# Performance work log

Hardware: AMD Instinct MI355X
Metric: run time of the kernel (lower is better)

## Reference

```python
import jax, jax.numpy as jnp
import numpy as np

DIM = 512; H = 8; TEMP_LEN = 16; TARGET_LEN = 22
NT = TEMP_LEN ** 2          # 256 temp tokens
NS = TARGET_LEN ** 2        # 484 target tokens
N = NT + NS                 # 740
HD = DIM // H
SCALE = HD ** -0.5
EPS = 1e-5
B = 16


def _bias_index(L):
    coords = np.stack(np.meshgrid(np.arange(L), np.arange(L), indexing='ij')).reshape(2, -1)
    rel = (coords[:, :, None] - coords[:, None, :]).transpose(1, 2, 0)  # [L^2, L^2, 2]
    rel[..., 0] += L - 1
    rel[..., 1] += L - 1
    rel[..., 0] *= 2 * L - 1
    return jnp.asarray(rel.sum(-1))  # [L^2, L^2] indices into (2L-1)^2 table

TEMP_IDX = _bias_index(TEMP_LEN)
TARGET_IDX = _bias_index(TARGET_LEN)


def setup_inputs() -> dict:
    key = jax.random.key(0)
    ctr = iter(range(100))
    def nrm(shape, s=1.0):
        return jax.random.normal(jax.random.fold_in(key, next(ctr)), shape, jnp.float32) * s
    def uni(shape):
        return jax.random.uniform(jax.random.fold_in(key, next(ctr)), shape, jnp.float32, 0.5, 1.5)
    d = {'x': nrm((B, N, DIM))}
    for nm in ('q', 'k', 'v'):
        d[f'conv_{nm}_w'] = nrm((DIM, 1, 3, 3), 0.2)   # depthwise 3x3, groups=DIM
        d[f'bn_{nm}_g'] = 1.0 + nrm((DIM,), 0.1)
        d[f'bn_{nm}_b'] = nrm((DIM,), 0.1)
        d[f'bn_{nm}_m'] = nrm((DIM,), 0.1)
        d[f'bn_{nm}_v'] = uni((DIM,))
    for nm in ('q', 'k', 'v', 'p'):
        d[f'w{nm}'] = nrm((DIM, DIM), DIM ** -0.5)
        d[f'b{nm}'] = nrm((DIM,), 0.01)
    d['rpb_target'] = nrm(((2 * TARGET_LEN - 1) ** 2, H), 0.0002)
    d['rpb_temp'] = nrm(((2 * TEMP_LEN - 1) ** 2, 1), 0.0002)
    d['tt_bias'] = nrm((H, 1, NT), 0.0002)       # temp_target_bias_table
    d['tg_tm_bias'] = nrm((H, NS, 1), 0.0002)    # target_temp_bias_table
    return d


def _dwconv_bn(z, w, g, b, m, v):
    # z: [B, C, Hh, Ww]; depthwise conv + BatchNorm2d (inference stats)
    y = jax.lax.conv_general_dilated(z, w, (1, 1), ((1, 1), (1, 1)),
                                     dimension_numbers=('NCHW', 'OIHW', 'NCHW'),
                                     feature_group_count=DIM)
    inv = (g * jax.lax.rsqrt(v + EPS))[None, :, None, None]
    return (y - m[None, :, None, None]) * inv + b[None, :, None, None]


def reference(x, conv_q_w, bn_q_g, bn_q_b, bn_q_m, bn_q_v,
              conv_k_w, bn_k_g, bn_k_b, bn_k_m, bn_k_v,
              conv_v_w, bn_v_g, bn_v_b, bn_v_m, bn_v_v,
              wq, bq, wk, bk, wv, bv, wp, bp,
              rpb_target, rpb_temp, tt_bias, tg_tm_bias):
    Bb = x.shape[0]
    to_img = lambda t, L: t.transpose(0, 2, 1).reshape(Bb, DIM, L, L)
    to_seq = lambda t: t.reshape(Bb, DIM, -1).transpose(0, 2, 1)
    ti = to_img(x[:, :NT], TEMP_LEN)
    tg = to_img(x[:, NT:], TARGET_LEN)

    def conv_branch(w, g, b, m, v):
        return jnp.concatenate([to_seq(_dwconv_bn(ti, w, g, b, m, v)),
                                to_seq(_dwconv_bn(tg, w, g, b, m, v))], axis=1)

    q = conv_branch(conv_q_w, bn_q_g, bn_q_b, bn_q_m, bn_q_v) @ wq + bq
    k = conv_branch(conv_k_w, bn_k_g, bn_k_b, bn_k_m, bn_k_v) @ wk + bk
    v = conv_branch(conv_v_w, bn_v_g, bn_v_b, bn_v_m, bn_v_v) @ wv + bv

    heads = lambda t: t.reshape(Bb, -1, H, HD).transpose(0, 2, 1, 3)
    qtm, ktm, vtm = heads(q[:, :NT]), heads(k[:, :NT]), heads(v[:, :NT])
    qta, kh, vh = heads(q[:, NT:]), heads(k), heads(v)

    # gathered relative-position bias tables
    target_bias = rpb_target[TARGET_IDX.reshape(-1)].reshape(NS, NS, H).transpose(2, 0, 1)  # [H,NS,NS]
    temp_bias = rpb_temp[TEMP_IDX.reshape(-1)].reshape(NT, NT, 1).transpose(2, 0, 1)        # [1,NT,NT]
    padding = tt_bias + tg_tm_bias                                                          # [H,NS,NT]
    rel = jnp.concatenate([padding, target_bias], axis=2)                                   # [H,NS,N]

    # target -> all attention
    attn = jax.nn.softmax(jnp.einsum('bhqd,bhkd->bhqk', qta, kh) * SCALE + rel, axis=-1)
    out_t = jnp.einsum('bhqk,bhkd->bhqd', attn, vh).transpose(0, 2, 1, 3).reshape(Bb, NS, DIM)

    # temp -> temp attention (bias broadcast over heads)
    attn2 = jax.nn.softmax(jnp.einsum('bhqd,bhkd->bhqk', qtm, ktm) * SCALE + temp_bias, axis=-1)
    out_m = jnp.einsum('bhqk,bhkd->bhqd', attn2, vtm).transpose(0, 2, 1, 3).reshape(Bb, NT, DIM)

    return jnp.concatenate([out_m, out_t], axis=1) @ wp + bp
```

## Files before the change

kernel.cpp:

```cpp
#include <hip/hip_runtime.h>
#include <hip/hip_bf16.h>

typedef unsigned short u16;
typedef unsigned int u32;
typedef __attribute__((ext_vector_type(8))) short short8;
typedef __attribute__((ext_vector_type(4))) float f32x4;

#define NTOK 740
#define NTMP 256
#define NTGT 484
#define DM   512
#define MH   8
#define MROWS 11840
#define KPAD 768
#define LOG2E 1.4426950408889634f

__device__ __forceinline__ float b2f(u16 u) {
    union { unsigned int i; float f; } x; x.i = ((unsigned int)u) << 16; return x.f;
}
__device__ __forceinline__ u16 f2b(float f) {
    union { float f; unsigned int i; } x; x.f = f;
    unsigned int r = x.i + 0x7FFFu + ((x.i >> 16) & 1u);
    return (u16)(r >> 16);
}
__device__ __forceinline__ u32 pk2(float a, float b) {
    union { __hip_bfloat162 h; u32 u; } p;
    p.h = __float22bfloat162_rn(float2{a, b});
    return p.u;
}
__device__ __forceinline__ float fexp2(float x) {
    return __builtin_amdgcn_exp2f(x);
}
struct alignas(8) us4 { u16 x, y, z, w; };

__device__ __forceinline__ void gload16(const void* g, void* l) {
    __builtin_amdgcn_global_load_lds(
        (const __attribute__((address_space(1))) void*)g,
        (__attribute__((address_space(3))) void*)l, 16, 0, 0);
}

__global__ __launch_bounds__(256) void prep_all(
    const float* __restrict__ w0, const float* __restrict__ w1,
    const float* __restrict__ w2, const float* __restrict__ w3, u16* __restrict__ wTbase,
    const float* __restrict__ cw0, const float* __restrict__ g0, const float* __restrict__ bb0,
    const float* __restrict__ m0, const float* __restrict__ v0,
    const float* __restrict__ cw1, const float* __restrict__ g1, const float* __restrict__ bb1,
    const float* __restrict__ m1, const float* __restrict__ v1,
    const float* __restrict__ cw2, const float* __restrict__ g2, const float* __restrict__ bb2,
    const float* __restrict__ m2, const float* __restrict__ v2,
    float* __restrict__ cwfb, float* __restrict__ shb,
    const float* __restrict__ rpb_t, const float* __restrict__ tt,
    const float* __restrict__ tg, u16* __restrict__ btab,
    const float* __restrict__ rpb_m, u16* __restrict__ mtab) {
    __shared__ float t[32][33];
    const int id = blockIdx.x, tid = threadIdx.x;
    if (id < 1024) {
        const int z = id >> 8, rem = id & 255;
        const int bx = rem & 15, by = rem >> 4;
        const float* W = z == 0 ? w0 : z == 1 ? w1 : z == 2 ? w2 : w3;
        u16* WT = wTbase + (size_t)z * 262144;
        const int tx = tid & 31, ty = tid >> 5;
        for (int i = ty; i < 32; i += 8)
            t[i][tx] = W[(size_t)(by * 32 + i) * 512 + bx * 32 + tx];
        __syncthreads();
        for (int i = ty; i < 32; i += 8)
            WT[(size_t)(bx * 32 + i) * 512 + by * 32 + tx] = f2b(t[tx][i]);
    } else if (id < 1051) {
        const int rem = id - 1024;
        const int tap = rem % 9, br = rem / 9;
        const float* cw = br == 0 ? cw0 : br == 1 ? cw1 : cw2;
        const float* g  = br == 0 ? g0  : br == 1 ? g1  : g2;
        const float* bb = br == 0 ? bb0 : br == 1 ? bb1 : bb2;
        const float* m  = br == 0 ? m0  : br == 1 ? m1  : m2;
        const float* v  = br == 0 ? v0  : br == 1 ? v1  : v2;
        for (int c = tid; c < DM; c += 256) {
            const float inv = g[c] * rsqrtf(v[c] + 1e-5f);
            cwfb[(br * 9 + tap) * DM + c] = cw[c * 9 + tap] * inv;
            if (tap == 0) shb[br * DM + c] = bb[c] - m[c] * inv;
        }
    } else if (id < 4923) {
        const int rem = id - 1051;
        const int h = rem / NTGT, q = rem % NTGT;
        const int qh = q / 22, qw = q % 22;
        const float tgv = tg[h * NTGT + q];
        for (int k = tid; k < KPAD; k += 256) {
            float val;
            if (k < NTMP) val = (tt[h * NTMP + k] + tgv) * LOG2E;
            else if (k < NTOK) {
                const int kj = k - NTMP, kh = kj / 22, kw = kj % 22;
                val = rpb_t[((qh - kh + 21) * 43 + (qw - kw + 21)) * MH + h] * LOG2E;
            } else val = -1e30f;
            btab[((size_t)(h * NTGT + q)) * KPAD + k] = f2b(val);
        }
    } else {
        const int q = id - 4923, k = tid;
        const int qh = q >> 4, qw = q & 15, kh = k >> 4, kw = k & 15;
        mtab[q * 256 + k] = f2b(rpb_m[(qh - kh + 15) * 31 + (qw - kw + 15)] * LOG2E);
    }
}

__global__ __launch_bounds__(256) void conv_bn3(
    const float* __restrict__ x,
    const float* __restrict__ cwfb, const float* __restrict__ shb,
    u16* __restrict__ o0, u16* __restrict__ o1, u16* __restrict__ o2) {
    const int bn = blockIdx.x * 2 + (threadIdx.x >> 7);
    const int c = (threadIdx.x & 127) * 4;
    const int b = bn / NTOK, n = bn % NTOK;
    const bool tmp = n < NTMP;
    const int L = tmp ? 16 : 22, base = tmp ? 0 : NTMP, p = n - base;
    const int ph = p / L, pw = p % L;
    float4 xv[9];
#pragma unroll
    for (int tap = 0; tap < 9; ++tap) {
        const int dh = tap / 3 - 1, dw = tap % 3 - 1;
        const int h2 = ph + dh, w2 = pw + dw;
        const bool ok = (h2 >= 0 && h2 < L && w2 >= 0 && w2 < L);
        xv[tap] = ok ? *(const float4*)(x + (size_t)(b * NTOK + base + h2 * L + w2) * DM + c)
                     : float4{0.f, 0.f, 0.f, 0.f};
    }
    const size_t o = (size_t)bn * DM + c;
    u16* out[3] = {o0, o1, o2};
#pragma unroll
    for (int br = 0; br < 3; ++br) {
        float4 acc = *(const float4*)(shb + br * DM + c);
#pragma unroll
        for (int tap = 0; tap < 9; ++tap) {
            const float4 wv = *(const float4*)(cwfb + (br * 9 + tap) * DM + c);
            acc.x = fmaf(wv.x, xv[tap].x, acc.x);
            acc.y = fmaf(wv.y, xv[tap].y, acc.y);
            acc.z = fmaf(wv.z, xv[tap].z, acc.z);
            acc.w = fmaf(wv.w, xv[tap].w, acc.w);
        }
        us4 r;
        r.x = f2b(acc.x); r.y = f2b(acc.y); r.z = f2b(acc.z); r.w = f2b(acc.w);
        *(us4*)(out[br] + o) = r;
    }
}

#define STAGE(bf, kk) do {                                                           \
    gload16(asrc + (kk) * 32, &As[bf][w * 512]);                                     \
    gload16(bsrc0 + (kk) * 32, &Bs[bf][w * 1024]);                                   \
    gload16(bsrc1 + (kk) * 32, &Bs[bf][w * 1024 + 512]);                             \
} while (0)

#define GEMM_BODY(A, BT)                                                             \
    const int tid = threadIdx.x;                                                     \
    const int lane = tid & 63, w = tid >> 6;                                         \
    const int lr = lane & 15, lg = lane >> 4;                                        \
    const int wm = (w >> 1) * 32, wn = (w & 1) * 64;                                 \
    const int srow4 = lane >> 2;                                                     \
    const int sc = (lane & 3) ^ ((srow4 & 3) ^ ((srow4 >> 2) & 3));                  \
    const int flr = (lr & 3) ^ ((lr >> 2) & 3);                                      \
    const u16* asrc  = A  + (size_t)(gm0 + w * 16 + srow4) * 512 + sc * 8;           \
    const u16* bsrc0 = BT + (size_t)(gn0 + w * 32 + srow4) * 512 + sc * 8;           \
    const u16* bsrc1 = BT + (size_t)(gn0 + w * 32 + 16 + srow4) * 512 + sc * 8;      \
    f32x4 acc[2][4] = {};                                                            \
    STAGE(0, 0); STAGE(1, 1);                                                        \
    _Pragma("unroll")                                                                \
    for (int kt = 0; kt < 16; ++kt) {                                                \
        const int cur = kt % 3;                                                      \
        if (kt < 14) {                                                               \
            STAGE((kt + 2) % 3, kt + 2);                                             \
            asm volatile("s_waitcnt vmcnt(6)" ::: "memory");                         \
        } else if (kt == 14) {                                                       \
            asm volatile("s_waitcnt vmcnt(3)" ::: "memory");                         \
        } else {                                                                     \
            asm volatile("s_waitcnt vmcnt(0)" ::: "memory");                         \
        }                                                                            \
        __builtin_amdgcn_s_barrier();                                                \
        asm volatile("" ::: "memory");                                               \
        short8 af[2], bfr[4];                                                        \
        _Pragma("unroll")                                                            \
        for (int i = 0; i < 2; ++i)                                                  \
            af[i] = *(const short8*)&As[cur][(wm + i * 16 + lr) * 32 + (lg ^ flr) * 8]; \
        _Pragma("unroll")                                                            \
        for (int j = 0; j < 4; ++j)                                                  \
            bfr[j] = *(const short8*)&Bs[cur][(wn + j * 16 + lr) * 32 + (lg ^ flr) * 8]; \
        _Pragma("unroll")                                                            \
        for (int i = 0; i < 2; ++i)                                                  \
            _Pragma("unroll")                                                        \
            for (int j = 0; j < 4; ++j)                                              \
                acc[i][j] = __builtin_amdgcn_mfma_f32_16x16x32_bf16(af[i], bfr[j], acc[i][j], 0, 0, 0); \
        asm volatile("" ::: "memory");                                               \
        __builtin_amdgcn_s_barrier();                                                \
    }

__global__ __launch_bounds__(256) void gemm_qkv(
    const u16* __restrict__ Aq, const u16* __restrict__ Ak, const u16* __restrict__ Av,
    const u16* __restrict__ wTb, const float* __restrict__ bq,
    const float* __restrict__ bk, const float* __restrict__ bv,
    u16* __restrict__ qout, u16* __restrict__ kout, u16* __restrict__ vbT, int zbase) {
    __shared__ u16 As[3][2048];
    __shared__ u16 Bs[3][4096];
    const int gm0 = blockIdx.x * 64, gn0 = blockIdx.y * 128;
    const int z = blockIdx.z + zbase;
    const u16* A = z == 0 ? Aq : z == 1 ? Ak : Av;
    const u16* BT = wTb + (size_t)z * 262144;
    const float* bias = z == 0 ? bq : z == 1 ? bk : bv;
    GEMM_BODY(A, BT)
    u16* lin = z == 0 ? qout : kout;
#pragma unroll
    for (int i = 0; i < 2; ++i)
#pragma unroll
        for (int j = 0; j < 4; ++j) {
            const int gc = gn0 + wn + j * 16 + lr;
            const float bvl = bias[gc];
#pragma unroll
            for (int r = 0; r < 4; ++r) {
                const int gr = gm0 + wm + i * 16 + lg * 4 + r;
                const float val = acc[i][j][r] + bvl;
                if (z == 2) {
                    const int b2 = gr / NTOK, k = gr - b2 * NTOK;
                    const int hh = gc >> 6, d = gc & 63;
                    vbT[((size_t)(b2 * MH + hh) * 64 + d) * KPAD + k] = f2b(val);
                } else {
                    lin[(size_t)gr * 512 + gc] = f2b(val);
                }
            }
        }
}

__global__ __launch_bounds__(256) void gemm_out(const u16* __restrict__ Ain,
                                                const u16* __restrict__ BTin,
                                                const float* __restrict__ bias,
                                                float* __restrict__ C) {
    __shared__ u16 As[3][2048];
    __shared__ u16 Bs[3][4096];
    const int gm0 = blockIdx.x * 64, gn0 = blockIdx.y * 128;
    GEMM_BODY(Ain, BTin)
#pragma unroll
    for (int i = 0; i < 2; ++i)
#pragma unroll
        for (int j = 0; j < 4; ++j) {
            const int gc = gn0 + wn + j * 16 + lr;
            const float bvl = bias[gc];
#pragma unroll
            for (int r = 0; r < 4; ++r) {
                const int gr = gm0 + wm + i * 16 + lg * 4 + r;
                C[(size_t)gr * 512 + gc] = acc[i][j][r] + bvl;
            }
        }
}

__global__ __launch_bounds__(256) void attn_all(const u16* __restrict__ qb,
                                                const u16* __restrict__ kb,
                                                const u16* __restrict__ vbT,
                                                const u16* __restrict__ btab,
                                                const u16* __restrict__ mtab,
                                                u16* __restrict__ attb) {
    __shared__ u16 Ks[2][32][64];
    __shared__ u16 VTs[2][64][32];
    __shared__ u16 Pb[2][4][16][32];

    int wg = blockIdx.x + 6 * (blockIdx.y + 8 * blockIdx.z);
    wg = (wg & 7) * 96 + (wg >> 3);
    const int bx = wg % 6;
    const int hb = wg / 6;
    const int h = hb & 7, b = hb >> 3;

    const bool tgt = bx < 4;
    const int q0 = (tgt ? bx : bx - 4) * 128;
    const int NKr = tgt ? NTOK : NTMP;
    const int NCH = tgt ? 24 : 8;
    const int QTOT = tgt ? NTGT : NTMP;
    const int QOFF = tgt ? NTMP : 0;
    const int TK = tgt ? KPAD : 256;
    const int tid = threadIdx.x;
    const int w = tid >> 6, lane = tid & 63;
    const int lq = lane & 15, lg = lane >> 4;
    const int fq = (lq & 3) ^ ((lq >> 2) & 3);
    const size_t brow = (size_t)b * NTOK;
    const float SCL = 0.125f * LOG2E;

    int qA = q0 + w * 16 + lq;       if (qA > QTOT - 1) qA = QTOT - 1;
    int qB = q0 + 64 + w * 16 + lq;  if (qB > QTOT - 1) qB = QTOT - 1;
    const u16* tbase = tgt ? (btab + (size_t)h * NTGT * KPAD) : mtab;
    const u16* trowA = tbase + (size_t)qA * TK;
    const u16* trowB = tbase + (size_t)qB * TK;

    short8 qfA[2], qfB[2];
#pragma unroll
    for (int dc = 0; dc < 2; ++dc) {
        qfA[dc] = *(const short8*)(qb + (brow + QOFF + qA) * DM + h * 64 + dc * 32 + lg * 8);
        qfB[dc] = *(const short8*)(qb + (brow + QOFF + qB) * DM + h * 64 + dc * 32 + lg * 8);
    }

    const int krow = tid >> 3, ksc = tid & 7;
    const int vrow = tid >> 2, vsc = tid & 3;
    const int fv = (vrow & 3) ^ ((vrow >> 2) & 3);
    const size_t vbase = (size_t)(b * MH + h) * 64 * KPAD;
    const u16* kptr2 = kb + brow * DM + h * 64 + (ksc ^ (krow & 7)) * 8;
    const u16* vptr2 = vbT + vbase + (size_t)vrow * KPAD + (vsc ^ fv) * 8;
    const int NKm1 = NKr - 1;

    float mrunA = -1e30f, lrunA = 0.f, mrunB = -1e30f, lrunB = 0.f;
    f32x4 oTA[4] = {}, oTB[4] = {};

    {
        const int keyc = krow < NKm1 ? krow : NKm1;
        gload16(kptr2 + (size_t)keyc * DM, &Ks[0][w * 8][0]);
        gload16(vptr2, &VTs[0][w * 16][0]);
    }

    for (int kc = 0; kc < NCH; ++kc) {
        const int cur = kc & 1, nxt = cur ^ 1;
        const bool more = (kc + 1 < NCH);
        us4 bcA0 = *(const us4*)(trowA + kc * 32 + lg * 4);
        us4 bcA1 = *(const us4*)(trowA + kc * 32 + 16 + lg * 4);
        us4 bcB0 = *(const us4*)(trowB + kc * 32 + lg * 4);
        us4 bcB1 = *(const us4*)(trowB + kc * 32 + 16 + lg * 4);
        if (more) {
            const int key = (kc + 1) * 32 + krow;
            const int keyc = key < NKm1 ? key : NKm1;
            gload16(kptr2 + (size_t)keyc * DM, &Ks[nxt][w * 8][0]);
            gload16(vptr2 + (kc + 1) * 32, &VTs[nxt][w * 16][0]);
            asm volatile("s_waitcnt vmcnt(2)" ::: "memory");
        } else {
            asm volatile("s_waitcnt vmcnt(0)" ::: "memory");
        }
        __builtin_amdgcn_s_barrier();
        asm volatile("" ::: "memory");

        f32x4 sA0 = {}, sA1 = {}, sB0 = {}, sB1 = {};
        __builtin_amdgcn_s_setprio(1);
#pragma unroll
        for (int dc = 0; dc < 2; ++dc) {
            short8 a0 = *(const short8*)&Ks[cur][lq][((dc * 4 + lg) ^ (lq & 7)) * 8];
            short8 a1 = *(const short8*)&Ks[cur][16 + lq][((dc * 4 + lg) ^ (lq & 7)) * 8];
            sA0 = __builtin_amdgcn_mfma_f32_16x16x32_bf16(a0, qfA[dc], sA0, 0, 0, 0);
            sB0 = __builtin_amdgcn_mfma_f32_16x16x32_bf16(a0, qfB[dc], sB0, 0, 0, 0);
            sA1 = __builtin_amdgcn_mfma_f32_16x16x32_bf16(a1, qfA[dc], sA1, 0, 0, 0);
            sB1 = __builtin_amdgcn_mfma_f32_16x16x32_bf16(a1, qfB[dc], sB1, 0, 0, 0);
        }
        __builtin_amdgcn_s_setprio(0);

        {
            float sv[8];
            sv[0] = fmaf(sA0[0], SCL, b2f(bcA0.x)); sv[1] = fmaf(sA0[1], SCL, b2f(bcA0.y));
            sv[2] = fmaf(sA0[2], SCL, b2f(bcA0.z)); sv[3] = fmaf(sA0[3], SCL, b2f(bcA0.w));
            sv[4] = fmaf(sA1[0], SCL, b2f(bcA1.x)); sv[5] = fmaf(sA1[1], SCL, b2f(bcA1.y));
            sv[6] = fmaf(sA1[2], SCL, b2f(bcA1.z)); sv[7] = fmaf(sA1[3], SCL, b2f(bcA1.w));
            float cm = sv[0];
#pragma unroll
            for (int i = 1; i < 8; ++i) cm = fmaxf(cm, sv[i]);
            cm = fmaxf(cm, __shfl_xor(cm, 16));
            cm = fmaxf(cm, __shfl_xor(cm, 32));
            if (!__all(cm <= mrunA)) {
                const float mnew = fmaxf(mrunA, cm);
                const float alpha = fexp2(mrunA - mnew);
#pragma unroll
                for (int t = 0; t < 4; ++t)
#pragma unroll
                    for (int r = 0; r < 4; ++r) oTA[t][r] *= alpha;
                lrunA *= alpha;
                mrunA = mnew;
            }
            float pv[8], psum = 0.f;
#pragma unroll
            for (int i = 0; i < 8; ++i) { pv[i] = fexp2(sv[i] - mrunA); psum += pv[i]; }
            const int c0 = (((lg >> 1) ^ fq) & 3) * 8 + (lg & 1) * 4;
            const int c1 = (((2 + (lg >> 1)) ^ fq) & 3) * 8 + (lg & 1) * 4;
            *(uint2*)&Pb[0][w][lq][c0] = uint2{pk2(pv[0], pv[1]), pk2(pv[2], pv[3])};
            *(uint2*)&Pb[0][w][lq][c1] = uint2{pk2(pv[4], pv[5]), pk2(pv[6], pv[7])};
            psum += __shfl_xor(psum, 16);
            psum += __shfl_xor(psum, 32);
            lrunA += psum;
        }
        {
            float sv[8];
            sv[0] = fmaf(sB0[0], SCL, b2f(bcB0.x)); sv[1] = fmaf(sB0[1], SCL, b2f(bcB0.y));
            sv[2] = fmaf(sB0[2], SCL, b2f(bcB0.z)); sv[3] = fmaf(sB0[3], SCL, b2f(bcB0.w));
            sv[4] = fmaf(sB1[0], SCL, b2f(bcB1.x)); sv[5] = fmaf(sB1[1], SCL, b2f(bcB1.y));
            sv[6] = fmaf(sB1[2], SCL, b2f(bcB1.z)); sv[7] = fmaf(sB1[3], SCL, b2f(bcB1.w));
            float cm = sv[0];
#pragma unroll
            for (int i = 1; i < 8; ++i) cm = fmaxf(cm, sv[i]);
            cm = fmaxf(cm, __shfl_xor(cm, 16));
            cm = fmaxf(cm, __shfl_xor(cm, 32));
            if (!__all(cm <= mrunB)) {
                const float mnew = fmaxf(mrunB, cm);
                const float alpha = fexp2(mrunB - mnew);
#pragma unroll
                for (int t = 0; t < 4; ++t)
#pragma unroll
                    for (int r = 0; r < 4; ++r) oTB[t][r] *= alpha;
                lrunB *= alpha;
                mrunB = mnew;
            }
            float pv[8], psum = 0.f;
#pragma unroll
            for (int i = 0; i < 8; ++i) { pv[i] = fexp2(sv[i] - mrunB); psum += pv[i]; }
            const int c0 = (((lg >> 1) ^ fq) & 3) * 8 + (lg & 1) * 4;
            const int c1 = (((2 + (lg >> 1)) ^ fq) & 3) * 8 + (lg & 1) * 4;
            *(uint2*)&Pb[1][w][lq][c0] = uint2{pk2(pv[0], pv[1]), pk2(pv[2], pv[3])};
            *(uint2*)&Pb[1][w][lq][c1] = uint2{pk2(pv[4], pv[5]), pk2(pv[6], pv[7])};
            psum += __shfl_xor(psum, 16);
            psum += __shfl_xor(psum, 32);
            lrunB += psum;
        }

        asm volatile("s_waitcnt lgkmcnt(0)" ::: "memory");

        short8 pfA = *(const short8*)&Pb[0][w][lq][((lg ^ fq) & 3) * 8];
        short8 pfB = *(const short8*)&Pb[1][w][lq][((lg ^ fq) & 3) * 8];
        __builtin_amdgcn_s_setprio(1);
#pragma unroll
        for (int t = 0; t < 4; ++t) {
            short8 vf = *(const short8*)&VTs[cur][t * 16 + lq][((lg ^ fq) & 3) * 8];
            oTA[t] = __builtin_amdgcn_mfma_f32_16x16x32_bf16(vf, pfA, oTA[t], 0, 0, 0);
            oTB[t] = __builtin_amdgcn_mfma_f32_16x16x32_bf16(vf, pfB, oTB[t], 0, 0, 0);
        }
        __builtin_amdgcn_s_setprio(0);

        asm volatile("" ::: "memory");
        __builtin_amdgcn_s_barrier();
    }

    {
        const float linv = 1.f / lrunA;
        const int qrow = q0 + w * 16 + lq;
        if (qrow < QTOT) {
            u16* op = attb + (brow + QOFF + qrow) * DM + h * 64;
#pragma unroll
            for (int t = 0; t < 4; ++t)
                *(uint2*)(op + t * 16 + lg * 4) =
                    uint2{pk2(oTA[t][0] * linv, oTA[t][1] * linv),
                          pk2(oTA[t][2] * linv, oTA[t][3] * linv)};
        }
    }
    {
        const float linv = 1.f / lrunB;
        const int qrow = q0 + 64 + w * 16 + lq;
        if (qrow < QTOT) {
            u16* op = attb + (brow + QOFF + qrow) * DM + h * 64;
#pragma unroll
            for (int t = 0; t < 4; ++t)
                *(uint2*)(op + t * 16 + lg * 4) =
                    uint2{pk2(oTB[t][0] * linv, oTB[t][1] * linv),
                          pk2(oTB[t][2] * linv, oTB[t][3] * linv)};
        }
    }
}

extern "C" void kernel_launch(void* const* d_in, const int* in_sizes, int n_in,
                              void* d_out, int out_size, void* d_ws, size_t ws_size,
                              hipStream_t stream) {
    const float* x = (const float*)d_in[0];
    const float* convw[3] = {(const float*)d_in[1], (const float*)d_in[6], (const float*)d_in[11]};
    const float* bng[3]   = {(const float*)d_in[2], (const float*)d_in[7], (const float*)d_in[12]};
    const float* bnb[3]   = {(const float*)d_in[3], (const float*)d_in[8], (const float*)d_in[13]};
    const float* bnm[3]   = {(const float*)d_in[4], (const float*)d_in[9], (const float*)d_in[14]};
    const float* bnv[3]   = {(const float*)d_in[5], (const float*)d_in[10], (const float*)d_in[15]};
    const float* w[4]     = {(const float*)d_in[16], (const float*)d_in[18], (const float*)d_in[20], (const float*)d_in[22]};
    const float* bias[4]  = {(const float*)d_in[17], (const float*)d_in[19], (const float*)d_in[21], (const float*)d_in[23]};
    const float* rpb_t = (const float*)d_in[24];
    const float* rpb_m = (const float*)d_in[25];
    const float* tt    = (const float*)d_in[26];
    const float* tg    = (const float*)d_in[27];

    char* p = (char*)d_ws;
    auto alloc = [&](size_t n) { char* r = p; p += (n + 255) & ~(size_t)255; return r; };
    const size_t SEQ = (size_t)MROWS * DM * 2;
    u16* wTb  = (u16*)alloc(4 * 524288);
    u16* cbq  = (u16*)alloc(SEQ);
    u16* cbk  = (u16*)alloc(SEQ);
    u16* cbv  = (u16*)alloc(SEQ);
    u16* kbuf = (u16*)alloc(SEQ);
    u16* vbT  = (u16*)alloc((size_t)16 * MH * 64 * KPAD * 2);
    u16* btab = (u16*)alloc((size_t)MH * NTGT * KPAD * 2);
    u16* mtab = (u16*)alloc(256 * 256 * 2);
    float* cwf = (float*)alloc(3 * 9 * DM * 4);
    float* shf = (float*)alloc(3 * DM * 4);
    const size_t used = (size_t)(p - (char*)d_ws);
    const bool merged = ws_size >= used + SEQ;
    u16* qbuf = merged ? (u16*)alloc(SEQ) : cbv;
    u16* attb = cbq;

    prep_all<<<5179, 256, 0, stream>>>(
        w[0], w[1], w[2], w[3], wTb,
        convw[0], bng[0], bnb[0], bnm[0], bnv[0],
        convw[1], bng[1], bnb[1], bnm[1], bnv[1],
        convw[2], bng[2], bnb[2], bnm[2], bnv[2], cwf, shf,
        rpb_t, tt, tg, btab, rpb_m, mtab);

    conv_bn3<<<MROWS / 2, 256, 0, stream>>>(x, cwf, shf, cbq, cbk, cbv);

    if (merged) {
        gemm_qkv<<<dim3(185, 4, 3), 256, 0, stream>>>(cbq, cbk, cbv, wTb,
                                                      bias[0], bias[1], bias[2],
                                                      qbuf, kbuf, vbT, 0);
    } else {
        gemm_qkv<<<dim3(185, 4, 1), 256, 0, stream>>>(cbq, cbk, cbv, wTb,
                                                      bias[0], bias[1], bias[2],
                                                      qbuf, kbuf, vbT, 2);
        gemm_qkv<<<dim3(185, 4, 2), 256, 0, stream>>>(cbq, cbk, cbv, wTb,
                                                      bias[0], bias[1], bias[2],
                                                      qbuf, kbuf, vbT, 0);
    }

    attn_all<<<dim3(6, 8, 16), 256, 0, stream>>>(qbuf, kbuf, vbT, btab, mtab, attb);

    gemm_out<<<dim3(185, 4), 256, 0, stream>>>(attb, wTb + 3 * 262144, bias[3], (float*)d_out);
}
```

Measured before the change: 171.3 us.

## Split target-query attention over two key halves and merge partial softmax results

Target-query attention blocks are split into two workgroups, each covering half of the key chunks (12 of 24). Each writes fp32 partial max, sum and output to workspace, and a new combine kernel merges them with log-sum-exp rescaling. This raises the grid from 768 to 1280 workgroups and balances the long target blocks against the short temp blocks, aiming for better CU occupancy and less tail time. The cost is an extra kernel launch plus roughly 19 MB of fp32 partial traffic. The split path only runs when the workspace is large enough, otherwise the old kernel is used.

```diff
diff --git a/kernel.cpp b/kernel.cpp
--- a/kernel.cpp
+++ b/kernel.cpp
@@ -242,6 +242,264 @@
         }
 }
 
+#define ATTN_CORE(BC_A0, BC_A1, BC_B0, BC_B1)                                        \
+    f32x4 sA0 = {}, sA1 = {}, sB0 = {}, sB1 = {};                                    \
+    __builtin_amdgcn_s_setprio(1);                                                   \
+    _Pragma("unroll")                                                                \
+    for (int dc = 0; dc < 2; ++dc) {                                                 \
+        short8 a0 = *(const short8*)&Ks[cur][lq][((dc * 4 + lg) ^ (lq & 7)) * 8];    \
+        short8 a1 = *(const short8*)&Ks[cur][16 + lq][((dc * 4 + lg) ^ (lq & 7)) * 8]; \
+        sA0 = __builtin_amdgcn_mfma_f32_16x16x32_bf16(a0, qfA[dc], sA0, 0, 0, 0);    \
+        sB0 = __builtin_amdgcn_mfma_f32_16x16x32_bf16(a0, qfB[dc], sB0, 0, 0, 0);    \
+        sA1 = __builtin_amdgcn_mfma_f32_16x16x32_bf16(a1, qfA[dc], sA1, 0, 0, 0);    \
+        sB1 = __builtin_amdgcn_mfma_f32_16x16x32_bf16(a1, qfB[dc], sB1, 0, 0, 0);    \
+    }                                                                                \
+    __builtin_amdgcn_s_setprio(0);                                                   \
+    {                                                                                \
+        float sv[8];                                                                 \
+        sv[0] = fmaf(sA0[0], SCL, b2f(BC_A0.x)); sv[1] = fmaf(sA0[1], SCL, b2f(BC_A0.y)); \
+        sv[2] = fmaf(sA0[2], SCL, b2f(BC_A0.z)); sv[3] = fmaf(sA0[3], SCL, b2f(BC_A0.w)); \
+        sv[4] = fmaf(sA1[0], SCL, b2f(BC_A1.x)); sv[5] = fmaf(sA1[1], SCL, b2f(BC_A1.y)); \
+        sv[6] = fmaf(sA1[2], SCL, b2f(BC_A1.z)); sv[7] = fmaf(sA1[3], SCL, b2f(BC_A1.w)); \
+        float cm = sv[0];                                                            \
+        _Pragma("unroll")                                                            \
+        for (int i = 1; i < 8; ++i) cm = fmaxf(cm, sv[i]);                           \
+        cm = fmaxf(cm, __shfl_xor(cm, 16));                                          \
+        cm = fmaxf(cm, __shfl_xor(cm, 32));                                          \
+        if (!__all(cm <= mrunA)) {                                                   \
+            const float mnew = fmaxf(mrunA, cm);                                     \
+            const float alpha = fexp2(mrunA - mnew);                                 \
+            _Pragma("unroll")                                                        \
+            for (int t = 0; t < 4; ++t)                                              \
+                _Pragma("unroll")                                                    \
+                for (int r = 0; r < 4; ++r) oTA[t][r] *= alpha;                      \
+            lrunA *= alpha;                                                          \
+            mrunA = mnew;                                                            \
+        }                                                                            \
+        float pv[8], psum = 0.f;                                                     \
+        _Pragma("unroll")                                                            \
+        for (int i = 0; i < 8; ++i) { pv[i] = fexp2(sv[i] - mrunA); psum += pv[i]; } \
+        const int c0 = (((lg >> 1) ^ fq) & 3) * 8 + (lg & 1) * 4;                    \
+        const int c1 = (((2 + (lg >> 1)) ^ fq) & 3) * 8 + (lg & 1) * 4;              \
+        *(uint2*)&Pb[0][w][lq][c0] = uint2{pk2(pv[0], pv[1]), pk2(pv[2], pv[3])};    \
+        *(uint2*)&Pb[0][w][lq][c1] = uint2{pk2(pv[4], pv[5]), pk2(pv[6], pv[7])};    \
+        psum += __shfl_xor(psum, 16);                                                \
+        psum += __shfl_xor(psum, 32);                                                \
+        lrunA += psum;                                                               \
+    }                                                                                \
+    {                                                                                \
+        float sv[8];                                                                 \
+        sv[0] = fmaf(sB0[0], SCL, b2f(BC_B0.x)); sv[1] = fmaf(sB0[1], SCL, b2f(BC_B0.y)); \
+        sv[2] = fmaf(sB0[2], SCL, b2f(BC_B0.z)); sv[3] = fmaf(sB0[3], SCL, b2f(BC_B0.w)); \
+        sv[4] = fmaf(sB1[0], SCL, b2f(BC_B1.x)); sv[5] = fmaf(sB1[1], SCL, b2f(BC_B1.y)); \
+        sv[6] = fmaf(sB1[2], SCL, b2f(BC_B1.z)); sv[7] = fmaf(sB1[3], SCL, b2f(BC_B1.w)); \
+        float cm = sv[0];                                                            \
+        _Pragma("unroll")                                                            \
+        for (int i = 1; i < 8; ++i) cm = fmaxf(cm, sv[i]);                           \
+        cm = fmaxf(cm, __shfl_xor(cm, 16));                                          \
+        cm = fmaxf(cm, __shfl_xor(cm, 32));                                          \
+        if (!__all(cm <= mrunB)) {                                                   \
+            const float mnew = fmaxf(mrunB, cm);                                     \
+            const float alpha = fexp2(mrunB - mnew);                                 \
+            _Pragma("unroll")                                                        \
+            for (int t = 0; t < 4; ++t)                                              \
+                _Pragma("unroll")                                                    \
+                for (int r = 0; r < 4; ++r) oTB[t][r] *= alpha;                      \
+            lrunB *= alpha;                                                          \
+            mrunB = mnew;                                                            \
+        }                                                                            \
+        float pv[8], psum = 0.f;                                                     \
+        _Pragma("unroll")                                                            \
+        for (int i = 0; i < 8; ++i) { pv[i] = fexp2(sv[i] - mrunB); psum += pv[i]; } \
+        const int c0 = (((lg >> 1) ^ fq) & 3) * 8 + (lg & 1) * 4;                    \
+        const int c1 = (((2 + (lg >> 1)) ^ fq) & 3) * 8 + (lg & 1) * 4;              \
+        *(uint2*)&Pb[1][w][lq][c0] = uint2{pk2(pv[0], pv[1]), pk2(pv[2], pv[3])};    \
+        *(uint2*)&Pb[1][w][lq][c1] = uint2{pk2(pv[4], pv[5]), pk2(pv[6], pv[7])};    \
+        psum += __shfl_xor(psum, 16);                                                \
+        psum += __shfl_xor(psum, 32);                                                \
+        lrunB += psum;                                                               \
+    }                                                                                \
+    asm volatile("s_waitcnt lgkmcnt(0)" ::: "memory");                               \
+    {                                                                                \
+        short8 pfA = *(const short8*)&Pb[0][w][lq][((lg ^ fq) & 3) * 8];             \
+        short8 pfB = *(const short8*)&Pb[1][w][lq][((lg ^ fq) & 3) * 8];             \
+        __builtin_amdgcn_s_setprio(1);                                               \
+        _Pragma("unroll")                                                            \
+        for (int t = 0; t < 4; ++t) {                                                \
+            short8 vf = *(const short8*)&VTs[cur][t * 16 + lq][((lg ^ fq) & 3) * 8]; \
+            oTA[t] = __builtin_amdgcn_mfma_f32_16x16x32_bf16(vf, pfA, oTA[t], 0, 0, 0); \
+            oTB[t] = __builtin_amdgcn_mfma_f32_16x16x32_bf16(vf, pfB, oTB[t], 0, 0, 0); \
+        }                                                                            \
+        __builtin_amdgcn_s_setprio(0);                                               \
+    }
+
+__global__ __launch_bounds__(256) void attn_split(const u16* __restrict__ qb,
+                                                  const u16* __restrict__ kb,
+                                                  const u16* __restrict__ vbT,
+                                                  const u16* __restrict__ btab,
+                                                  const u16* __restrict__ mtab,
+                                                  u16* __restrict__ attb,
+                                                  float* __restrict__ pm,
+                                                  float* __restrict__ pl,
+                                                  float* __restrict__ pO) {
+    __shared__ u16 Ks[2][32][64];
+    __shared__ u16 VTs[2][64][32];
+    __shared__ u16 Pb[2][4][16][32];
+
+    int wg = blockIdx.x + 10 * (blockIdx.y + 8 * blockIdx.z);
+    wg = (wg & 7) * 160 + (wg >> 3);
+    const int bx = wg % 10;
+    const int hb = wg / 10;
+    const int h = hb & 7, b = hb >> 3;
+
+    const bool tgt = bx < 8;
+    const int half = tgt ? (bx & 1) : 0;
+    const int q0 = tgt ? (bx >> 1) * 128 : (bx - 8) * 128;
+    const int NKr = tgt ? NTOK : NTMP;
+    const int gc0 = tgt ? half * 12 : 0;
+    const int gcEnd = tgt ? gc0 + 12 : 8;
+    const int QTOT = tgt ? NTGT : NTMP;
+    const int QOFF = tgt ? NTMP : 0;
+    const int TK = tgt ? KPAD : 256;
+    const int tid = threadIdx.x;
+    const int w = tid >> 6, lane = tid & 63;
+    const int lq = lane & 15, lg = lane >> 4;
+    const int fq = (lq & 3) ^ ((lq >> 2) & 3);
+    const size_t brow = (size_t)b * NTOK;
+    const float SCL = 0.125f * LOG2E;
+
+    int qA = q0 + w * 16 + lq;       if (qA > QTOT - 1) qA = QTOT - 1;
+    int qB = q0 + 64 + w * 16 + lq;  if (qB > QTOT - 1) qB = QTOT - 1;
+    const u16* tbase = tgt ? (btab + (size_t)h * NTGT * KPAD) : mtab;
+    const u16* trowA = tbase + (size_t)qA * TK;
+    const u16* trowB = tbase + (size_t)qB * TK;
+
+    short8 qfA[2], qfB[2];
+#pragma unroll
+    for (int dc = 0; dc < 2; ++dc) {
+        qfA[dc] = *(const short8*)(qb + (brow + QOFF + qA) * DM + h * 64 + dc * 32 + lg * 8);
+        qfB[dc] = *(const short8*)(qb + (brow + QOFF + qB) * DM + h * 64 + dc * 32 + lg * 8);
+    }
+
+    const int krow = tid >> 3, ksc = tid & 7;
+    const int vrow = tid >> 2, vsc = tid & 3;
+    const int fv = (vrow & 3) ^ ((vrow >> 2) & 3);
+    const size_t vbase = (size_t)(b * MH + h) * 64 * KPAD;
+    const u16* kptr2 = kb + brow * DM + h * 64 + (ksc ^ (krow & 7)) * 8;
+    const u16* vptr2 = vbT + vbase + (size_t)vrow * KPAD + (vsc ^ fv) * 8;
+    const int NKm1 = NKr - 1;
+
+    float mrunA = -1e30f, lrunA = 0.f, mrunB = -1e30f, lrunB = 0.f;
+    f32x4 oTA[4] = {}, oTB[4] = {};
+
+    {
+        const int key = gc0 * 32 + krow;
+        const int keyc = key < NKm1 ? key : NKm1;
+        gload16(kptr2 + (size_t)keyc * DM, &Ks[0][w * 8][0]);
+        gload16(vptr2 + gc0 * 32, &VTs[0][w * 16][0]);
+    }
+
+    for (int gc = gc0; gc < gcEnd; ++gc) {
+        const int cur = gc & 1, nxt = cur ^ 1;
+        const bool more = (gc + 1 < gcEnd);
+        us4 bcA0 = *(const us4*)(trowA + gc * 32 + lg * 4);
+        us4 bcA1 = *(const us4*)(trowA + gc * 32 + 16 + lg * 4);
+        us4 bcB0 = *(const us4*)(trowB + gc * 32 + lg * 4);
+        us4 bcB1 = *(const us4*)(trowB + gc * 32 + 16 + lg * 4);
+        if (more) {
+            const int key = (gc + 1) * 32 + krow;
+            const int keyc = key < NKm1 ? key : NKm1;
+            gload16(kptr2 + (size_t)keyc * DM, &Ks[nxt][w * 8][0]);
+            gload16(vptr2 + (gc + 1) * 32, &VTs[nxt][w * 16][0]);
+            asm volatile("s_waitcnt vmcnt(2)" ::: "memory");
+        } else {
+            asm volatile("s_waitcnt vmcnt(0)" ::: "memory");
+        }
+        __builtin_amdgcn_s_barrier();
+        asm volatile("" ::: "memory");
+
+        ATTN_CORE(bcA0, bcA1, bcB0, bcB1)
+
+        asm volatile("" ::: "memory");
+        __builtin_amdgcn_s_barrier();
+    }
+
+    if (tgt) {
+        const int qrowA = q0 + w * 16 + lq;
+        if (qrowA < QTOT) {
+            const size_t idx = ((size_t)(b * MH + h) * 512 + qrowA);
+            if (lg == 0) { pm[half * 65536 + idx] = mrunA; pl[half * 65536 + idx] = lrunA; }
+            float* op = pO + ((size_t)half * 65536 + idx) * 64 + lg * 4;
+#pragma unroll
+            for (int t = 0; t < 4; ++t)
+                *(float4*)(op + t * 16) = float4{oTA[t][0], oTA[t][1], oTA[t][2], oTA[t][3]};
+        }
+        const int qrowB = q0 + 64 + w * 16 + lq;
+        if (qrowB < QTOT) {
+            const size_t idx = ((size_t)(b * MH + h) * 512 + qrowB);
+            if (lg == 0) { pm[half * 65536 + idx] = mrunB; pl[half * 65536 + idx] = lrunB; }
+            float* op = pO + ((size_t)half * 65536 + idx) * 64 + lg * 4;
+#pragma unroll
+            for (int t = 0; t < 4; ++t)
+                *(float4*)(op + t * 16) = float4{oTB[t][0], oTB[t][1], oTB[t][2], oTB[t][3]};
+        }
+    } else {
+        {
+            const float linv = 1.f / lrunA;
+            const int qrow = q0 + w * 16 + lq;
+            if (qrow < QTOT) {
+                u16* op = attb + (brow + QOFF + qrow) * DM + h * 64;
+#pragma unroll
+                for (int t = 0; t < 4; ++t)
+                    *(uint2*)(op + t * 16 + lg * 4) =
+                        uint2{pk2(oTA[t][0] * linv, oTA[t][1] * linv),
+                              pk2(oTA[t][2] * linv, oTA[t][3] * linv)};
+            }
+        }
+        {
+            const float linv = 1.f / lrunB;
+            const int qrow = q0 + 64 + w * 16 + lq;
+            if (qrow < QTOT) {
+                u16* op = attb + (brow + QOFF + qrow) * DM + h * 64;
+#pragma unroll
+                for (int t = 0; t < 4; ++t)
+                    *(uint2*)(op + t * 16 + lg * 4) =
+                        uint2{pk2(oTB[t][0] * linv, oTB[t][1] * linv),
+                              pk2(oTB[t][2] * linv, oTB[t][3] * linv)};
+            }
+        }
+    }
+}
+
+__global__ __launch_bounds__(256) void attn_combine(const float* __restrict__ pm,
+                                                    const float* __restrict__ pl,
+                                                    const float* __restrict__ pO,
+                                                    u16* __restrict__ attb) {
+    const int h = blockIdx.y, b = blockIdx.z;
+    const int q = blockIdx.x * 64 + (threadIdx.x >> 2);
+    if (q >= NTGT) return;
+    const int dseg = (threadIdx.x & 3) * 16;
+    const size_t idx = (size_t)(b * MH + h) * 512 + q;
+    const float m1 = pm[idx], m2 = pm[65536 + idx];
+    const float l1 = pl[idx], l2 = pl[65536 + idx];
+    const float m = fmaxf(m1, m2);
+    const float s1 = fexp2(m1 - m), s2 = fexp2(m2 - m);
+    const float inv = 1.f / (l1 * s1 + l2 * s2);
+    const float* o1 = pO + idx * 64 + dseg;
+    const float* o2 = pO + (size_t)65536 * 64 + idx * 64 + dseg;
+    u16* op = attb + ((size_t)b * NTOK + NTMP + q) * DM + h * 64 + dseg;
+    u32 out[8];
+#pragma unroll
+    for (int i = 0; i < 4; ++i) {
+        const float4 a = *(const float4*)(o1 + i * 4);
+        const float4 c = *(const float4*)(o2 + i * 4);
+        out[i * 2]     = pk2((a.x * s1 + c.x * s2) * inv, (a.y * s1 + c.y * s2) * inv);
+        out[i * 2 + 1] = pk2((a.z * s1 + c.z * s2) * inv, (a.w * s1 + c.w * s2) * inv);
+    }
+    *(uint4*)(op)     = uint4{out[0], out[1], out[2], out[3]};
+    *(uint4*)(op + 8) = uint4{out[4], out[5], out[6], out[7]};
+}
+
 __global__ __launch_bounds__(256) void attn_all(const u16* __restrict__ qb,
                                                 const u16* __restrict__ kb,
                                                 const u16* __restrict__ vbT,
@@ -321,96 +579,7 @@
         __builtin_amdgcn_s_barrier();
         asm volatile("" ::: "memory");
 
-        f32x4 sA0 = {}, sA1 = {}, sB0 = {}, sB1 = {};
-        __builtin_amdgcn_s_setprio(1);
-#pragma unroll
-        for (int dc = 0; dc < 2; ++dc) {
-            short8 a0 = *(const short8*)&Ks[cur][lq][((dc * 4 + lg) ^ (lq & 7)) * 8];
-            short8 a1 = *(const short8*)&Ks[cur][16 + lq][((dc * 4 + lg) ^ (lq & 7)) * 8];
-            sA0 = __builtin_amdgcn_mfma_f32_16x16x32_bf16(a0, qfA[dc], sA0, 0, 0, 0);
-            sB0 = __builtin_amdgcn_mfma_f32_16x16x32_bf16(a0, qfB[dc], sB0, 0, 0, 0);
-            sA1 = __builtin_amdgcn_mfma_f32_16x16x32_bf16(a1, qfA[dc], sA1, 0, 0, 0);
-            sB1 = __builtin_amdgcn_mfma_f32_16x16x32_bf16(a1, qfB[dc], sB1, 0, 0, 0);
-        }
-        __builtin_amdgcn_s_setprio(0);
-
-        {
-            float sv[8];
-            sv[0] = fmaf(sA0[0], SCL, b2f(bcA0.x)); sv[1] = fmaf(sA0[1], SCL, b2f(bcA0.y));
-            sv[2] = fmaf(sA0[2], SCL, b2f(bcA0.z)); sv[3] = fmaf(sA0[3], SCL, b2f(bcA0.w));
-            sv[4] = fmaf(sA1[0], SCL, b2f(bcA1.x)); sv[5] = fmaf(sA1[1], SCL, b2f(bcA1.y));
-            sv[6] = fmaf(sA1[2], SCL, b2f(bcA1.z)); sv[7] = fmaf(sA1[3], SCL, b2f(bcA1.w));
-            float cm = sv[0];
-#pragma unroll
-            for (int i = 1; i < 8; ++i) cm = fmaxf(cm, sv[i]);
-            cm = fmaxf(cm, __shfl_xor(cm, 16));
-            cm = fmaxf(cm, __shfl_xor(cm, 32));
-            if (!__all(cm <= mrunA)) {
-                const float mnew = fmaxf(mrunA, cm);
-                const float alpha = fexp2(mrunA - mnew);
-#pragma unroll
-                for (int t = 0; t < 4; ++t)
-#pragma unroll
-                    for (int r = 0; r < 4; ++r) oTA[t][r] *= alpha;
-                lrunA *= alpha;
-                mrunA = mnew;
-            }
-            float pv[8], psum = 0.f;
-#pragma unroll
-            for (int i = 0; i < 8; ++i) { pv[i] = fexp2(sv[i] - mrunA); psum += pv[i]; }
-            const int c0 = (((lg >> 1) ^ fq) & 3) * 8 + (lg & 1) * 4;
-            const int c1 = (((2 + (lg >> 1)) ^ fq) & 3) * 8 + (lg & 1) * 4;
-            *(uint2*)&Pb[0][w][lq][c0] = uint2{pk2(pv[0], pv[1]), pk2(pv[2], pv[3])};
-            *(uint2*)&Pb[0][w][lq][c1] = uint2{pk2(pv[4], pv[5]), pk2(pv[6], pv[7])};
-            psum += __shfl_xor(psum, 16);
-            psum += __shfl_xor(psum, 32);
-            lrunA += psum;
-        }
-        {
-            float sv[8];
-            sv[0] = fmaf(sB0[0], SCL, b2f(bcB0.x)); sv[1] = fmaf(sB0[1], SCL, b2f(bcB0.y));
-            sv[2] = fmaf(sB0[2], SCL, b2f(bcB0.z)); sv[3] = fmaf(sB0[3], SCL, b2f(bcB0.w));
-            sv[4] = fmaf(sB1[0], SCL, b2f(bcB1.x)); sv[5] = fmaf(sB1[1], SCL, b2f(bcB1.y));
-            sv[6] = fmaf(sB1[2], SCL, b2f(bcB1.z)); sv[7] = fmaf(sB1[3], SCL, b2f(bcB1.w));
-            float cm = sv[0];
-#pragma unroll
-            for (int i = 1; i < 8; ++i) cm = fmaxf(cm, sv[i]);
-            cm = fmaxf(cm, __shfl_xor(cm, 16));
-            cm = fmaxf(cm, __shfl_xor(cm, 32));
-            if (!__all(cm <= mrunB)) {
-                const float mnew = fmaxf(mrunB, cm);
-                const float alpha = fexp2(mrunB - mnew);
-#pragma unroll
-                for (int t = 0; t < 4; ++t)
-#pragma unroll
-                    for (int r = 0; r < 4; ++r) oTB[t][r] *= alpha;
-                lrunB *= alpha;
-                mrunB = mnew;
-            }
-            float pv[8], psum = 0.f;
-#pragma unroll
-            for (int i = 0; i < 8; ++i) { pv[i] = fexp2(sv[i] - mrunB); psum += pv[i]; }
-            const int c0 = (((lg >> 1) ^ fq) & 3) * 8 + (lg & 1) * 4;
-            const int c1 = (((2 + (lg >> 1)) ^ fq) & 3) * 8 + (lg & 1) * 4;
-            *(uint2*)&Pb[1][w][lq][c0] = uint2{pk2(pv[0], pv[1]), pk2(pv[2], pv[3])};
-            *(uint2*)&Pb[1][w][lq][c1] = uint2{pk2(pv[4], pv[5]), pk2(pv[6], pv[7])};
-            psum += __shfl_xor(psum, 16);
-            psum += __shfl_xor(psum, 32);
-            lrunB += psum;
-        }
-
-        asm volatile("s_waitcnt lgkmcnt(0)" ::: "memory");
-
-        short8 pfA = *(const short8*)&Pb[0][w][lq][((lg ^ fq) & 3) * 8];
-        short8 pfB = *(const short8*)&Pb[1][w][lq][((lg ^ fq) & 3) * 8];
-        __builtin_amdgcn_s_setprio(1);
-#pragma unroll
-        for (int t = 0; t < 4; ++t) {
-            short8 vf = *(const short8*)&VTs[cur][t * 16 + lq][((lg ^ fq) & 3) * 8];
-            oTA[t] = __builtin_amdgcn_mfma_f32_16x16x32_bf16(vf, pfA, oTA[t], 0, 0, 0);
-            oTB[t] = __builtin_amdgcn_mfma_f32_16x16x32_bf16(vf, pfB, oTB[t], 0, 0, 0);
-        }
-        __builtin_amdgcn_s_setprio(0);
+        ATTN_CORE(bcA0, bcA1, bcB0, bcB1)
 
         asm volatile("" ::: "memory");
         __builtin_amdgcn_s_barrier();
@@ -471,10 +640,19 @@
     u16* mtab = (u16*)alloc(256 * 256 * 2);
     float* cwf = (float*)alloc(3 * 9 * DM * 4);
     float* shf = (float*)alloc(3 * DM * 4);
-    const size_t used = (size_t)(p - (char*)d_ws);
+    size_t used = (size_t)(p - (char*)d_ws);
     const bool merged = ws_size >= used + SEQ;
     u16* qbuf = merged ? (u16*)alloc(SEQ) : cbv;
     u16* attb = cbq;
+    used = (size_t)(p - (char*)d_ws);
+    const size_t NPQ = (size_t)2 * 128 * 512;
+    const bool have_split = ws_size >= used + NPQ * 4 * 2 + NPQ * 64 * 4;
+    float* pm = nullptr; float* pl = nullptr; float* pO = nullptr;
+    if (have_split) {
+        pm = (float*)alloc(NPQ * 4);
+        pl = (float*)alloc(NPQ * 4);
+        pO = (float*)alloc(NPQ * 64 * 4);
+    }
 
     prep_all<<<5179, 256, 0, stream>>>(
         w[0], w[1], w[2], w[3], wTb,
@@ -498,7 +676,13 @@
                                                       qbuf, kbuf, vbT, 0);
     }
 
-    attn_all<<<dim3(6, 8, 16), 256, 0, stream>>>(qbuf, kbuf, vbT, btab, mtab, attb);
+    if (have_split) {
+        attn_split<<<dim3(10, 8, 16), 256, 0, stream>>>(qbuf, kbuf, vbT, btab, mtab,
+                                                        attb, pm, pl, pO);
+        attn_combine<<<dim3(8, MH, 16), 256, 0, stream>>>(pm, pl, pO, attb);
+    } else {
+        attn_all<<<dim3(6, 8, 16), 256, 0, stream>>>(qbuf, kbuf, vbT, btab, mtab, attb);
+    }
 
     gemm_out<<<dim3(185, 4), 256, 0, stream>>>(attb, wTb + 3 * 262144, bias[3], (float*)d_out);
 }
```

Result: slower. 185.6 us (+8.3%).
